# Kernel tuning notes

Hardware: AMD Instinct MI355X
Metric: run time of the kernel (lower is better)

The kernel has to match this reference:

```python
import jax, jax.numpy as jnp
import numpy as np

B, T, D = 4, 4096, 1024
H, E, K, SPAN = 16, 8, 2, 64
GATE_H = 128


def setup_inputs() -> dict:
    key = jax.random.key(0)
    ks = jax.random.split(key, 7)
    s = 0.02
    return {
        "hidden_states": jax.random.normal(ks[0], (B, T, D), jnp.float32),
        "attention_mask": jnp.ones((B, T), jnp.int32),
        # expert weights, torch Linear convention: y = x @ W.T, W: (out, in)
        "Wq": jax.random.normal(ks[1], (E, D, D), jnp.float32) * s,
        "Wk": jax.random.normal(ks[2], (E, D, D), jnp.float32) * s,
        "Wv": jax.random.normal(ks[3], (E, D, D), jnp.float32) * s,
        "gate_w1": jax.random.normal(ks[4], (GATE_H, D), jnp.float32) * s,
        "gate_b1": jnp.zeros((GATE_H,), jnp.float32),
        "gate_w2": jax.random.normal(ks[5], (E, GATE_H), jnp.float32) * s,
        "gate_b2": jnp.zeros((E,), jnp.float32),
    }


def reference(hidden_states, attention_mask, Wq, Wk, Wv, gate_w1, gate_b1, gate_w2, gate_b2):
    b, t, c = hidden_states.shape
    n_spans = t // SPAN  # T divisible by span_len, full mask -> even split
    hd = c // H
    x = hidden_states.reshape(b, n_spans, SPAN, c)            # (B,S,L,C)
    m = attention_mask.reshape(b, n_spans, SPAN).astype(jnp.float32)

    # masked mean-pool per span
    pooled = (x * m[..., None]).sum(2) / jnp.clip(m.sum(2), 1e-9)[..., None]  # (B,S,C)

    # gating MLP + top-k sparse softmax weights
    h = jax.nn.relu(pooled @ gate_w1.T + gate_b1)
    logits = h @ gate_w2.T + gate_b2                          # (B,S,E)
    vals, idx = jax.lax.top_k(logits, K)
    sm = jax.nn.softmax(vals, axis=-1)
    gw = (jax.nn.one_hot(idx, E, dtype=sm.dtype) * sm[..., None]).sum(-2)  # (B,S,E)

    def combine(W):
        # sum_j gw[...,j] * (x @ W_j.T); small fixed loop over experts
        out = jnp.zeros_like(x)
        for j in range(E):
            out = out + gw[:, :, j][:, :, None, None] * jnp.einsum('bsld,fd->bslf', x, W[j])
        return out

    def heads(z):
        return z.reshape(b, n_spans, SPAN, H, hd).transpose(0, 1, 3, 2, 4)  # (B,S,H,L,hd)

    Qh = heads(combine(Wq))
    Kh = heads(combine(Wk))
    Vh = heads(combine(Wv))

    scores = jnp.einsum('bshld,bshmd->bshlm', Qh, Kh) / jnp.sqrt(jnp.float32(hd))
    mb = (m > 0)[:, :, None, None, :]                         # mask keys
    scores = jnp.where(mb, scores, jnp.finfo(scores.dtype).min)
    probs = jax.nn.softmax(scores, axis=-1)                    # dropout=0 (eval)
    ctx = jnp.einsum('bshlm,bshmd->bshld', probs, Vh)
    out = ctx.transpose(0, 1, 3, 2, 4).reshape(b, t, c)
    return out
```

## Files before the change

### kernel.cpp

```cpp
#include <hip/hip_runtime.h>
#include <hip/hip_bf16.h>
#include <hip/hip_fp16.h>

constexpr int Bc = 4, Tc = 4096, Dc = 1024, Hc = 16, Ec = 8;
constexpr int SPANc = 64, NSc = 64, HDc = 64, GHc = 128;
constexpr int NSPAN = 256;
constexpr int MAXMT = 134;
constexpr int NTILES = 12;
#define FINF_MIN (-3.402823466e38f)

typedef __attribute__((ext_vector_type(8))) _Float16 half8;
typedef __attribute__((ext_vector_type(4))) _Float16 half4;
typedef __attribute__((ext_vector_type(4))) float f32x4;

#define LD4(p) (*reinterpret_cast<const float4*>(p))
#define LDU4(p) (*reinterpret_cast<const uint4*>(p))
#define MFMA16(A, B, C) __builtin_amdgcn_mfma_f32_16x16x32_f16(A, B, C, 0, 0, 0)

constexpr size_t OFF_EIDX = 0;
constexpr size_t OFF_EGW  = 2048;
constexpr size_t OFF_NMT  = 6144;
constexpr size_t OFF_MT   = 6208;
constexpr size_t OFF_UT   = 65536;
constexpr size_t UT_BYTES = (size_t)NSPAN * 2 * 3072 * 64 * 2;
constexpr size_t WS_MID   = OFF_UT + UT_BYTES;
constexpr size_t OFF_W16  = WS_MID;
constexpr size_t W16_BYTES = (size_t)3 * Ec * Dc * Dc * 2;
constexpr size_t WS_W16   = OFF_W16 + W16_BYTES;

__global__ __launch_bounds__(256) void cvt16_kernel(
    const float* __restrict__ src, _Float16* __restrict__ dst, int n8, float scl)
{
  int i = blockIdx.x * 256 + threadIdx.x;
  const int stride = gridDim.x * 256;
  for (; i < n8; i += stride) {
    const float4 a = LD4(src + (size_t)i * 8);
    const float4 b = LD4(src + (size_t)i * 8 + 4);
    half8 h;
    h[0] = (_Float16)(a.x * scl); h[1] = (_Float16)(a.y * scl);
    h[2] = (_Float16)(a.z * scl); h[3] = (_Float16)(a.w * scl);
    h[4] = (_Float16)(b.x * scl); h[5] = (_Float16)(b.y * scl);
    h[6] = (_Float16)(b.z * scl); h[7] = (_Float16)(b.w * scl);
    *reinterpret_cast<half8*>(dst + (size_t)i * 8) = h;
  }
}

__global__ __launch_bounds__(256) void gate_kernel(
    const float* __restrict__ x, const int* __restrict__ mask,
    const float* __restrict__ w1, const float* __restrict__ b1,
    const float* __restrict__ w2, const float* __restrict__ b2,
    int* __restrict__ eidx, float* __restrict__ egw)
{
  const int span = blockIdx.x;
  const int b = span / NSc, s = span % NSc;
  const int tid = threadIdx.x;

  __shared__ float mv[SPANc];
  __shared__ float msum_s;
  __shared__ float pooled[Dc];
  __shared__ float hbuf[GHc];
  __shared__ float logits[Ec];

  if (tid < SPANc) mv[tid] = (float)mask[(size_t)b * Tc + s * SPANc + tid];
  __syncthreads();
  if (tid == 0) {
    float ms = 0.f;
    for (int l = 0; l < SPANc; ++l) ms += mv[l];
    msum_s = fmaxf(ms, 1e-9f);
  }
  __syncthreads();

  {
    const int c0 = tid * 4;
    float a0 = 0.f, a1 = 0.f, a2 = 0.f, a3 = 0.f;
    const float* xb = x + ((size_t)b * Tc + s * SPANc) * Dc + c0;
    for (int l = 0; l < SPANc; ++l) {
      const float m = mv[l];
      const float4 v = *reinterpret_cast<const float4*>(xb + (size_t)l * Dc);
      a0 += v.x * m; a1 += v.y * m; a2 += v.z * m; a3 += v.w * m;
    }
    const float inv = 1.f / msum_s;
    pooled[c0 + 0] = a0 * inv; pooled[c0 + 1] = a1 * inv;
    pooled[c0 + 2] = a2 * inv; pooled[c0 + 3] = a3 * inv;
  }
  __syncthreads();

  if (tid < GHc) {
    const float* wr = w1 + (size_t)tid * Dc;
    float acc = b1[tid];
    for (int c = 0; c < Dc; c += 4) {
      const float4 w = *reinterpret_cast<const float4*>(wr + c);
      acc += pooled[c] * w.x + pooled[c + 1] * w.y + pooled[c + 2] * w.z + pooled[c + 3] * w.w;
    }
    hbuf[tid] = fmaxf(acc, 0.f);
  }
  __syncthreads();

  if (tid < Ec) {
    const float* wr = w2 + tid * GHc;
    float acc = b2[tid];
    for (int j = 0; j < GHc; ++j) acc += hbuf[j] * wr[j];
    logits[tid] = acc;
  }
  __syncthreads();

  if (tid == 0) {
    int e0 = 0; float v0 = logits[0];
    for (int e = 1; e < Ec; ++e) { if (logits[e] > v0) { v0 = logits[e]; e0 = e; } }
    int e1 = (e0 == 0) ? 1 : 0; float v1 = logits[e1];
    for (int e = 0; e < Ec; ++e) {
      if (e == e0 || e == e1) continue;
      if (logits[e] > v1) { v1 = logits[e]; e1 = e; }
    }
    const float ex = expf(v1 - v0);
    const float den = 1.f + ex;
    eidx[span * 2 + 0] = e0; eidx[span * 2 + 1] = e1;
    egw[span * 2 + 0] = 1.f / den; egw[span * 2 + 1] = ex / den;
  }
}

__global__ __launch_bounds__(64) void bookkeep_kernel(
    const int* __restrict__ eidx, int* __restrict__ nmt, int* __restrict__ mtiles)
{
  __shared__ int codes[Ec][NSPAN * 2];
  __shared__ int cnt[Ec];
  __shared__ int base[Ec + 1];
  const int tid = threadIdx.x;

  if (tid < Ec) {
    int c = 0;
    for (int s = 0; s < NSPAN; ++s) {
      for (int j = 0; j < 2; ++j) {
        if (eidx[s * 2 + j] == tid) codes[tid][c++] = s * 2 + j;
      }
    }
    cnt[tid] = c;
  }
  __syncthreads();
  if (tid == 0) {
    int acc = 0;
    for (int e = 0; e < Ec; ++e) { base[e] = acc; acc += (cnt[e] + 3) >> 2; }
    base[Ec] = acc;
    *nmt = acc;
  }
  __syncthreads();
  if (tid < Ec) {
    const int e = tid, c = cnt[e], ng = (c + 3) >> 2;
    for (int g = 0; g < ng; ++g) {
      const int m = base[e] + g;
      mtiles[m * 8 + 0] = e;
      for (int i = 0; i < 4; ++i) {
        const int li = g * 4 + i;
        mtiles[m * 8 + 1 + i] = codes[e][(li < c) ? li : 0];
      }
    }
  }
}

__global__ __launch_bounds__(512, 2) void moe_gemm_w16(
    const float* __restrict__ x, const _Float16* __restrict__ W16,
    const int* __restrict__ nmt, const int* __restrict__ mtiles,
    _Float16* __restrict__ Ut)
{
  const int lin = blockIdx.x + gridDim.x * blockIdx.y;
  const int lin2 = (lin & 7) * 201 + (lin >> 3);
  const int mt = lin2 % MAXMT;
  const int nt = lin2 / MAXMT;
  if (mt >= *nmt) return;

  const int e = mtiles[mt * 8 + 0];
  int codes[4];
#pragma unroll
  for (int i = 0; i < 4; ++i) codes[i] = mtiles[mt * 8 + 1 + i];

  const int mat = nt >> 2;
  const int wcol0 = (nt & 3) * 256;
  const _Float16* Wb = W16 + (size_t)mat * ((size_t)Ec * Dc * Dc)
                     + ((size_t)e * Dc + wcol0) * Dc;

  __shared__ _Float16 As[256][36];
  __shared__ _Float16 Bs[256][36];

  const int t = threadIdx.x;
  const int arow = t >> 1;
  const int acol0 = (t & 1) * 16;
  const float* asrc =
      x + ((size_t)(codes[arow >> 6] >> 1) * SPANc + (arow & 63)) * Dc + acol0;
  const _Float16* bsrc = Wb + (size_t)arow * Dc + acol0;

  const int w = t >> 6, lane = t & 63;
  const int lr = lane & 15, koff = (lane >> 4) * 8;
  const int rbase = (w >> 2) * 128;
  const int cbase = (w & 3) * 64;

  f32x4 acc[8][4];
#pragma unroll
  for (int ri = 0; ri < 8; ++ri)
#pragma unroll
    for (int ci = 0; ci < 4; ++ci)
#pragma unroll
      for (int j = 0; j < 4; ++j) acc[ri][ci][j] = 0.f;

  float4 pa0 = LD4(asrc), pa1 = LD4(asrc + 4), pa2 = LD4(asrc + 8), pa3 = LD4(asrc + 12);
  uint4 pb0 = LDU4(bsrc), pb1 = LDU4(bsrc + 8);

  for (int k0 = 0; k0 < Dc; k0 += 32) {
    __syncthreads();
    {
      half8 ha;
      ha[0] = (_Float16)pa0.x; ha[1] = (_Float16)pa0.y;
      ha[2] = (_Float16)pa0.z; ha[3] = (_Float16)pa0.w;
      ha[4] = (_Float16)pa1.x; ha[5] = (_Float16)pa1.y;
      ha[6] = (_Float16)pa1.z; ha[7] = (_Float16)pa1.w;
      *reinterpret_cast<half8*>(&As[arow][acol0]) = ha;
      ha[0] = (_Float16)pa2.x; ha[1] = (_Float16)pa2.y;
      ha[2] = (_Float16)pa2.z; ha[3] = (_Float16)pa2.w;
      ha[4] = (_Float16)pa3.x; ha[5] = (_Float16)pa3.y;
      ha[6] = (_Float16)pa3.z; ha[7] = (_Float16)pa3.w;
      *reinterpret_cast<half8*>(&As[arow][acol0 + 8]) = ha;
      *reinterpret_cast<uint4*>(&Bs[arow][acol0]) = pb0;
      *reinterpret_cast<uint4*>(&Bs[arow][acol0 + 8]) = pb1;
    }
    if (k0 < Dc - 32) {
      asrc += 32; bsrc += 32;
      pa0 = LD4(asrc); pa1 = LD4(asrc + 4); pa2 = LD4(asrc + 8); pa3 = LD4(asrc + 12);
      pb0 = LDU4(bsrc); pb1 = LDU4(bsrc + 8);
      __builtin_amdgcn_sched_barrier(0);
    }
    __syncthreads();

    half8 afr[8], bfr[4];
#pragma unroll
    for (int ri = 0; ri < 8; ++ri)
      afr[ri] = *reinterpret_cast<const half8*>(&As[rbase + ri * 16 + lr][koff]);
#pragma unroll
    for (int ci = 0; ci < 4; ++ci)
      bfr[ci] = *reinterpret_cast<const half8*>(&Bs[cbase + ci * 16 + lr][koff]);
    __builtin_amdgcn_s_setprio(1);
#pragma unroll
    for (int ri = 0; ri < 8; ++ri)
#pragma unroll
      for (int ci = 0; ci < 4; ++ci)
        acc[ri][ci] = MFMA16(afr[ri], bfr[ci], acc[ri][ci]);
    __builtin_amdgcn_s_setprio(0);
  }

#pragma unroll
  for (int ri = 0; ri < 8; ++ri)
#pragma unroll
    for (int ci = 0; ci < 4; ++ci) {
      const int f = wcol0 + cbase + ci * 16 + lr;
      const int row0 = rbase + ri * 16 + (lane >> 4) * 4;
      const int slot = codes[row0 >> 6];
      half4 hv;
#pragma unroll
      for (int j = 0; j < 4; ++j) hv[j] = (_Float16)acc[ri][ci][j];
      *reinterpret_cast<half4*>(
          Ut + ((size_t)slot * 3072 + mat * 1024 + f) * 64 + (row0 & 63)) = hv;
    }
}

__global__ __launch_bounds__(512, 2) void moe_gemm_f32(
    const float* __restrict__ x,
    const float* __restrict__ Wq, const float* __restrict__ Wk,
    const float* __restrict__ Wv,
    const int* __restrict__ nmt, const int* __restrict__ mtiles,
    _Float16* __restrict__ Ut)
{
  const int lin = blockIdx.x + gridDim.x * blockIdx.y;
  const int lin2 = (lin & 7) * 201 + (lin >> 3);
  const int mt = lin2 % MAXMT;
  const int nt = lin2 / MAXMT;
  if (mt >= *nmt) return;

  const int e = mtiles[mt * 8 + 0];
  int codes[4];
#pragma unroll
  for (int i = 0; i < 4; ++i) codes[i] = mtiles[mt * 8 + 1 + i];

  const int mat = nt >> 2;
  const int wcol0 = (nt & 3) * 256;
  const float* Wp = (mat == 0) ? Wq : (mat == 1) ? Wk : Wv;
  const float* Wbase = Wp + ((size_t)e * Dc + wcol0) * Dc;

  __shared__ _Float16 As[256][36];
  __shared__ _Float16 Bs[256][36];

  const int t = threadIdx.x;
  const int arow = t >> 1;
  const int acol0 = (t & 1) * 16;
  const float* asrc =
      x + ((size_t)(codes[arow >> 6] >> 1) * SPANc + (arow & 63)) * Dc + acol0;
  const float* bsrc = Wbase + (size_t)arow * Dc + acol0;

  const int w = t >> 6, lane = t & 63;
  const int lr = lane & 15, koff = (lane >> 4) * 8;
  const int rbase = (w >> 2) * 128;
  const int cbase = (w & 3) * 64;

  f32x4 acc[8][4];
#pragma unroll
  for (int ri = 0; ri < 8; ++ri)
#pragma unroll
    for (int ci = 0; ci < 4; ++ci)
#pragma unroll
      for (int j = 0; j < 4; ++j) acc[ri][ci][j] = 0.f;

  float4 pa0 = LD4(asrc), pa1 = LD4(asrc + 4), pa2 = LD4(asrc + 8), pa3 = LD4(asrc + 12);
  float4 pb0 = LD4(bsrc), pb1 = LD4(bsrc + 4), pb2 = LD4(bsrc + 8), pb3 = LD4(bsrc + 12);

  for (int k0 = 0; k0 < Dc; k0 += 32) {
    __syncthreads();
    {
      half8 ha, hb;
      ha[0] = (_Float16)pa0.x; ha[1] = (_Float16)pa0.y;
      ha[2] = (_Float16)pa0.z; ha[3] = (_Float16)pa0.w;
      ha[4] = (_Float16)pa1.x; ha[5] = (_Float16)pa1.y;
      ha[6] = (_Float16)pa1.z; ha[7] = (_Float16)pa1.w;
      *reinterpret_cast<half8*>(&As[arow][acol0]) = ha;
      ha[0] = (_Float16)pa2.x; ha[1] = (_Float16)pa2.y;
      ha[2] = (_Float16)pa2.z; ha[3] = (_Float16)pa2.w;
      ha[4] = (_Float16)pa3.x; ha[5] = (_Float16)pa3.y;
      ha[6] = (_Float16)pa3.z; ha[7] = (_Float16)pa3.w;
      *reinterpret_cast<half8*>(&As[arow][acol0 + 8]) = ha;
      hb[0] = (_Float16)(pb0.x * 64.f); hb[1] = (_Float16)(pb0.y * 64.f);
      hb[2] = (_Float16)(pb0.z * 64.f); hb[3] = (_Float16)(pb0.w * 64.f);
      hb[4] = (_Float16)(pb1.x * 64.f); hb[5] = (_Float16)(pb1.y * 64.f);
      hb[6] = (_Float16)(pb1.z * 64.f); hb[7] = (_Float16)(pb1.w * 64.f);
      *reinterpret_cast<half8*>(&Bs[arow][acol0]) = hb;
      hb[0] = (_Float16)(pb2.x * 64.f); hb[1] = (_Float16)(pb2.y * 64.f);
      hb[2] = (_Float16)(pb2.z * 64.f); hb[3] = (_Float16)(pb2.w * 64.f);
      hb[4] = (_Float16)(pb3.x * 64.f); hb[5] = (_Float16)(pb3.y * 64.f);
      hb[6] = (_Float16)(pb3.z * 64.f); hb[7] = (_Float16)(pb3.w * 64.f);
      *reinterpret_cast<half8*>(&Bs[arow][acol0 + 8]) = hb;
    }
    if (k0 < Dc - 32) {
      asrc += 32; bsrc += 32;
      pa0 = LD4(asrc); pa1 = LD4(asrc + 4); pa2 = LD4(asrc + 8); pa3 = LD4(asrc + 12);
      pb0 = LD4(bsrc); pb1 = LD4(bsrc + 4); pb2 = LD4(bsrc + 8); pb3 = LD4(bsrc + 12);
      __builtin_amdgcn_sched_barrier(0);
    }
    __syncthreads();

    half8 afr[8], bfr[4];
#pragma unroll
    for (int ri = 0; ri < 8; ++ri)
      afr[ri] = *reinterpret_cast<const half8*>(&As[rbase + ri * 16 + lr][koff]);
#pragma unroll
    for (int ci = 0; ci < 4; ++ci)
      bfr[ci] = *reinterpret_cast<const half8*>(&Bs[cbase + ci * 16 + lr][koff]);
#pragma unroll
    for (int ri = 0; ri < 8; ++ri)
#pragma unroll
      for (int ci = 0; ci < 4; ++ci)
        acc[ri][ci] = MFMA16(afr[ri], bfr[ci], acc[ri][ci]);
  }

#pragma unroll
  for (int ri = 0; ri < 8; ++ri)
#pragma unroll
    for (int ci = 0; ci < 4; ++ci) {
      const int f = wcol0 + cbase + ci * 16 + lr;
      const int row0 = rbase + ri * 16 + (lane >> 4) * 4;
      const int slot = codes[row0 >> 6];
      half4 hv;
#pragma unroll
      for (int j = 0; j < 4; ++j) hv[j] = (_Float16)acc[ri][ci][j];
      *reinterpret_cast<half4*>(
          Ut + ((size_t)slot * 3072 + mat * 1024 + f) * 64 + (row0 & 63)) = hv;
    }
}

__global__ __launch_bounds__(256, 3) void attn_kernel(
    const int* __restrict__ mask, const float* __restrict__ egw,
    const _Float16* __restrict__ Ut, float* __restrict__ out)
{
  const int h = blockIdx.x;
  const int s = blockIdx.y;
  const int b = blockIdx.z;
  const int span = b * NSc + s;
  const int tid = threadIdx.x;

  __shared__ _Float16 Qf[64][68];
  __shared__ _Float16 Kf[64][68];
  __shared__ _Float16 VT[64][68];
  __shared__ _Float16 Pf[64][68];
  __shared__ float    sc[64][68];

  const int sA = span * 2 + 0;
  const int sB = span * 2 + 1;
  const float gA = egw[span * 2 + 0] * 0.015625f;
  const float gB = egw[span * 2 + 1] * 0.015625f;

  const int d = tid >> 2;
  const int l0 = (tid & 3) * 16;

  for (int mat = 0; mat < 3; ++mat) {
    const _Float16* pa = Ut + ((size_t)sA * 3072 + mat * 1024 + h * HDc + d) * 64 + l0;
    const _Float16* pb = Ut + ((size_t)sB * 3072 + mat * 1024 + h * HDc + d) * 64 + l0;
    const half8 a0 = *reinterpret_cast<const half8*>(pa);
    const half8 a1 = *reinterpret_cast<const half8*>(pa + 8);
    const half8 b0 = *reinterpret_cast<const half8*>(pb);
    const half8 b1 = *reinterpret_cast<const half8*>(pb + 8);
    if (mat == 2) {
      half8 v0, v1;
#pragma unroll
      for (int j = 0; j < 8; ++j) {
        v0[j] = (_Float16)(gA * (float)a0[j] + gB * (float)b0[j]);
        v1[j] = (_Float16)(gA * (float)a1[j] + gB * (float)b1[j]);
      }
      *reinterpret_cast<half8*>(&VT[d][l0]) = v0;
      *reinterpret_cast<half8*>(&VT[d][l0 + 8]) = v1;
    } else if (mat == 0) {
#pragma unroll
      for (int j = 0; j < 8; ++j) {
        Qf[l0 + j][d] = (_Float16)(gA * (float)a0[j] + gB * (float)b0[j]);
        Qf[l0 + 8 + j][d] = (_Float16)(gA * (float)a1[j] + gB * (float)b1[j]);
      }
    } else {
#pragma unroll
      for (int j = 0; j < 8; ++j) {
        Kf[l0 + j][d] = (_Float16)(gA * (float)a0[j] + gB * (float)b0[j]);
        Kf[l0 + 8 + j][d] = (_Float16)(gA * (float)a1[j] + gB * (float)b1[j]);
      }
    }
  }
  __syncthreads();

  const int w = tid >> 6, lane = tid & 63;
  const int lr = lane & 15, koff = (lane >> 4) * 8;
  const int rbase = (w >> 1) * 32, cbase = (w & 1) * 32;

  {
    f32x4 aS[2][2];
#pragma unroll
    for (int mi = 0; mi < 2; ++mi)
#pragma unroll
      for (int ni = 0; ni < 2; ++ni)
#pragma unroll
        for (int j = 0; j < 4; ++j) aS[mi][ni][j] = 0.f;
#pragma unroll
    for (int kc = 0; kc < 64; kc += 32) {
      const half8 a0 = *reinterpret_cast<const half8*>(&Qf[rbase + lr][kc + koff]);
      const half8 a1 = *reinterpret_cast<const half8*>(&Qf[rbase + 16 + lr][kc + koff]);
      const half8 b0 = *reinterpret_cast<const half8*>(&Kf[cbase + lr][kc + koff]);
      const half8 b1 = *reinterpret_cast<const half8*>(&Kf[cbase + 16 + lr][kc + koff]);
      aS[0][0] = MFMA16(a0, b0, aS[0][0]); aS[0][1] = MFMA16(a0, b1, aS[0][1]);
      aS[1][0] = MFMA16(a1, b0, aS[1][0]); aS[1][1] = MFMA16(a1, b1, aS[1][1]);
    }
    const bool kv0 = mask[(size_t)b * Tc + s * SPANc + cbase + lr] != 0;
    const bool kv1 = mask[(size_t)b * Tc + s * SPANc + cbase + 16 + lr] != 0;
#pragma unroll
    for (int mi = 0; mi < 2; ++mi)
#pragma unroll
      for (int ni = 0; ni < 2; ++ni) {
        const int col = cbase + ni * 16 + lr;
        const int row0 = rbase + mi * 16 + (lane >> 4) * 4;
        const bool kv = (ni == 0) ? kv0 : kv1;
#pragma unroll
        for (int j = 0; j < 4; ++j)
          sc[row0 + j][col] = kv ? aS[mi][ni][j] * 0.125f : FINF_MIN;
      }
  }
  __syncthreads();

  if (tid < 64) {
    float mx = FINF_MIN;
    for (int mm = 0; mm < 64; ++mm) {
      const int m = (mm + tid) & 63;
      mx = fmaxf(mx, sc[tid][m]);
    }
    float sum = 0.f;
    for (int mm = 0; mm < 64; ++mm) {
      const int m = (mm + tid) & 63;
      const float e = expf(sc[tid][m] - mx);
      sc[tid][m] = e;
      sum += e;
    }
    const float inv = 1.f / sum;
    for (int mm = 0; mm < 64; ++mm) {
      const int m = (mm + tid) & 63;
      Pf[tid][m] = (_Float16)(sc[tid][m] * inv);
    }
  }
  __syncthreads();

  {
    f32x4 aC[2][2];
#pragma unroll
    for (int mi = 0; mi < 2; ++mi)
#pragma unroll
      for (int ni = 0; ni < 2; ++ni)
#pragma unroll
        for (int j = 0; j < 4; ++j) aC[mi][ni][j] = 0.f;
#pragma unroll
    for (int kc = 0; kc < 64; kc += 32) {
      const half8 a0 = *reinterpret_cast<const half8*>(&Pf[rbase + lr][kc + koff]);
      const half8 a1 = *reinterpret_cast<const half8*>(&Pf[rbase + 16 + lr][kc + koff]);
      const half8 b0 = *reinterpret_cast<const half8*>(&VT[cbase + lr][kc + koff]);
      const half8 b1 = *reinterpret_cast<const half8*>(&VT[cbase + 16 + lr][kc + koff]);
      aC[0][0] = MFMA16(a0, b0, aC[0][0]); aC[0][1] = MFMA16(a0, b1, aC[0][1]);
      aC[1][0] = MFMA16(a1, b0, aC[1][0]); aC[1][1] = MFMA16(a1, b1, aC[1][1]);
    }
    float* ob = out + ((size_t)b * Tc + s * SPANc) * Dc + h * HDc;
#pragma unroll
    for (int mi = 0; mi < 2; ++mi)
#pragma unroll
      for (int ni = 0; ni < 2; ++ni) {
        const int col = cbase + ni * 16 + lr;
        const int row0 = rbase + mi * 16 + (lane >> 4) * 4;
#pragma unroll
        for (int j = 0; j < 4; ++j)
          ob[(size_t)(row0 + j) * Dc + col] = aC[mi][ni][j];
      }
  }
}

__global__ __launch_bounds__(256, 3) void moe_attn_fb(
    const float* __restrict__ x, const int* __restrict__ mask,
    const float* __restrict__ Wq, const float* __restrict__ Wk,
    const float* __restrict__ Wv,
    const int* __restrict__ eidx, const float* __restrict__ egw,
    float* __restrict__ out)
{
  const int h = blockIdx.x;
  const int s = blockIdx.y;
  const int b = blockIdx.z;
  const int span = b * NSc + s;
  const int tid = threadIdx.x;

  __shared__ __align__(16) char smem[52224];
  _Float16* XF  = (_Float16*)(smem);
  _Float16* WHs = (_Float16*)(smem + 5120);
  _Float16* WLs = (_Float16*)(smem + 10240);
  float* qs = (float*)(smem);
  float* ks = (float*)(smem + 17408);
  float* vs = (float*)(smem + 34816);

  const int e0 = eidx[span * 2 + 0];
  const int e1 = eidx[span * 2 + 1];
  const float g0s = egw[span * 2 + 0] * 64.f;
  const float g1s = egw[span * 2 + 1] * 64.f;

  const int lrow = tid >> 2;
  const int kq = (tid & 3) * 8;
  const int stg_off = lrow * 40 + kq;

  const int w = tid >> 6;
  const int lane = tid & 63;
  const int lr = lane & 15;
  const int koff = (lane >> 4) * 8;
  const int rbase = (w >> 1) * 32;
  const int cbase = (w & 1) * 32;

  const float* xb = x + ((size_t)b * Tc + s * SPANc) * Dc;
  const size_t woff0 = ((size_t)e0 * Dc + h * HDc + lrow) * Dc + kq;
  const size_t woff1 = ((size_t)e1 * Dc + h * HDc + lrow) * Dc + kq;

  const float* xcur  = xb + (size_t)lrow * Dc + kq;
  const float* w0cur = Wv + woff0;
  const float* w1cur = Wv + woff1;
  float4 rx0, rx1, ra0, ra1, rb0, rb1;
  rx0 = LD4(xcur); rx1 = LD4(xcur + 4);
  ra0 = LD4(w0cur); ra1 = LD4(w0cur + 4);
  rb0 = LD4(w1cur); rb1 = LD4(w1cur + 4);

  for (int p = 0; p < 3; ++p) {
    f32x4 acc[2][2];
#pragma unroll
    for (int mi = 0; mi < 2; ++mi)
#pragma unroll
      for (int ni = 0; ni < 2; ++ni)
#pragma unroll
        for (int j = 0; j < 4; ++j) acc[mi][ni][j] = 0.f;

    for (int t = 0; t < 32; ++t) {
      __syncthreads();
      {
        half8 hx;
        hx[0] = (_Float16)rx0.x; hx[1] = (_Float16)rx0.y;
        hx[2] = (_Float16)rx0.z; hx[3] = (_Float16)rx0.w;
        hx[4] = (_Float16)rx1.x; hx[5] = (_Float16)rx1.y;
        hx[6] = (_Float16)rx1.z; hx[7] = (_Float16)rx1.w;
        *reinterpret_cast<half8*>(XF + stg_off) = hx;
      }
      {
        float wv[8];
        wv[0] = g0s * ra0.x + g1s * rb0.x; wv[1] = g0s * ra0.y + g1s * rb0.y;
        wv[2] = g0s * ra0.z + g1s * rb0.z; wv[3] = g0s * ra0.w + g1s * rb0.w;
        wv[4] = g0s * ra1.x + g1s * rb1.x; wv[5] = g0s * ra1.y + g1s * rb1.y;
        wv[6] = g0s * ra1.z + g1s * rb1.z; wv[7] = g0s * ra1.w + g1s * rb1.w;
        half8 hw, lw;
#pragma unroll
        for (int i = 0; i < 8; ++i) {
          const _Float16 wh = (_Float16)wv[i];
          hw[i] = wh;
          lw[i] = (_Float16)(wv[i] - (float)wh);
        }
        *reinterpret_cast<half8*>(WHs + stg_off) = hw;
        *reinterpret_cast<half8*>(WLs + stg_off) = lw;
      }
      if (!(p == 2 && t == 31)) {
        if (t < 31) {
          xcur += 32; w0cur += 32; w1cur += 32;
        } else {
          const float* Wn = (p == 0) ? Wk : Wq;
          xcur = xb + (size_t)lrow * Dc + kq;
          w0cur = Wn + woff0;
          w1cur = Wn + woff1;
        }
        rx0 = LD4(xcur); rx1 = LD4(xcur + 4);
        ra0 = LD4(w0cur); ra1 = LD4(w0cur + 4);
        rb0 = LD4(w1cur); rb1 = LD4(w1cur + 4);
      }
      __syncthreads();

      const half8 a0  = *reinterpret_cast<const half8*>(XF  + (rbase + lr) * 40 + koff);
      const half8 a1  = *reinterpret_cast<const half8*>(XF  + (rbase + 16 + lr) * 40 + koff);
      const half8 bh0 = *reinterpret_cast<const half8*>(WHs + (cbase + lr) * 40 + koff);
      const half8 bh1 = *reinterpret_cast<const half8*>(WHs + (cbase + 16 + lr) * 40 + koff);
      const half8 bl0 = *reinterpret_cast<const half8*>(WLs + (cbase + lr) * 40 + koff);
      const half8 bl1 = *reinterpret_cast<const half8*>(WLs + (cbase + 16 + lr) * 40 + koff);

      acc[0][0] = MFMA16(a0, bh0, acc[0][0]);
      acc[0][1] = MFMA16(a0, bh1, acc[0][1]);
      acc[1][0] = MFMA16(a1, bh0, acc[1][0]);
      acc[1][1] = MFMA16(a1, bh1, acc[1][1]);
      acc[0][0] = MFMA16(a0, bl0, acc[0][0]);
      acc[0][1] = MFMA16(a0, bl1, acc[0][1]);
      acc[1][0] = MFMA16(a1, bl0, acc[1][0]);
      acc[1][1] = MFMA16(a1, bl1, acc[1][1]);
    }

    float* dst = (p == 0) ? vs : (p == 1) ? ks : qs;
    if (p == 2) __syncthreads();
#pragma unroll
    for (int mi = 0; mi < 2; ++mi)
#pragma unroll
      for (int ni = 0; ni < 2; ++ni) {
        const int col = cbase + ni * 16 + lr;
        const int row0 = rbase + mi * 16 + (lane >> 4) * 4;
#pragma unroll
        for (int j = 0; j < 4; ++j)
          dst[(row0 + j) * 68 + col] = acc[mi][ni][j] * 0.015625f;
      }
  }
  __syncthreads();

  const int tx = tid & 15;
  const int ty = tid >> 4;
  bool kvalid[4];
#pragma unroll
  for (int j = 0; j < 4; ++j)
    kvalid[j] = mask[(size_t)b * Tc + s * SPANc + tx * 4 + j] != 0;

  float sacc[4][4] = {{0.f, 0.f, 0.f, 0.f}, {0.f, 0.f, 0.f, 0.f},
                      {0.f, 0.f, 0.f, 0.f}, {0.f, 0.f, 0.f, 0.f}};
  for (int dd = 0; dd < 64; ++dd) {
    const int d = (dd + tid) & 63;
    const float a0 = qs[(ty * 4 + 0) * 68 + d], a1 = qs[(ty * 4 + 1) * 68 + d];
    const float a2 = qs[(ty * 4 + 2) * 68 + d], a3 = qs[(ty * 4 + 3) * 68 + d];
    const float b0 = ks[(tx * 4 + 0) * 68 + d], b1v = ks[(tx * 4 + 1) * 68 + d];
    const float b2v = ks[(tx * 4 + 2) * 68 + d], b3 = ks[(tx * 4 + 3) * 68 + d];
    sacc[0][0] += a0 * b0; sacc[0][1] += a0 * b1v; sacc[0][2] += a0 * b2v; sacc[0][3] += a0 * b3;
    sacc[1][0] += a1 * b0; sacc[1][1] += a1 * b1v; sacc[1][2] += a1 * b2v; sacc[1][3] += a1 * b3;
    sacc[2][0] += a2 * b0; sacc[2][1] += a2 * b1v; sacc[2][2] += a2 * b2v; sacc[2][3] += a2 * b3;
    sacc[3][0] += a3 * b0; sacc[3][1] += a3 * b1v; sacc[3][2] += a3 * b2v; sacc[3][3] += a3 * b3;
  }
  __syncthreads();
#pragma unroll
  for (int i = 0; i < 4; ++i)
#pragma unroll
    for (int j = 0; j < 4; ++j)
      qs[(ty * 4 + i) * 68 + tx * 4 + j] = kvalid[j] ? sacc[i][j] * 0.125f : FINF_MIN;
  __syncthreads();

  if (tid < 64) {
    float mx = FINF_MIN;
    for (int mm = 0; mm < 64; ++mm) {
      const int m = (mm + tid) & 63;
      mx = fmaxf(mx, qs[tid * 68 + m]);
    }
    float sum = 0.f;
    for (int mm = 0; mm < 64; ++mm) {
      const int m = (mm + tid) & 63;
      const float e = expf(qs[tid * 68 + m] - mx);
      qs[tid * 68 + m] = e;
      sum += e;
    }
    const float inv = 1.f / sum;
    for (int mm = 0; mm < 64; ++mm) {
      const int m = (mm + tid) & 63;
      qs[tid * 68 + m] *= inv;
    }
  }
  __syncthreads();

  float cacc[4][4] = {{0.f, 0.f, 0.f, 0.f}, {0.f, 0.f, 0.f, 0.f},
                      {0.f, 0.f, 0.f, 0.f}, {0.f, 0.f, 0.f, 0.f}};
  for (int m = 0; m < 64; ++m) {
    const float p0 = qs[(ty * 4 + 0) * 68 + m], p1 = qs[(ty * 4 + 1) * 68 + m];
    const float p2 = qs[(ty * 4 + 2) * 68 + m], p3 = qs[(ty * 4 + 3) * 68 + m];
    const float4 vv = *reinterpret_cast<const float4*>(&vs[m * 68 + tx * 4]);
    cacc[0][0] += p0 * vv.x; cacc[0][1] += p0 * vv.y; cacc[0][2] += p0 * vv.z; cacc[0][3] += p0 * vv.w;
    cacc[1][0] += p1 * vv.x; cacc[1][1] += p1 * vv.y; cacc[1][2] += p1 * vv.z; cacc[1][3] += p1 * vv.w;
    cacc[2][0] += p2 * vv.x; cacc[2][1] += p2 * vv.y; cacc[2][2] += p2 * vv.z; cacc[2][3] += p2 * vv.w;
    cacc[3][0] += p3 * vv.x; cacc[3][1] += p3 * vv.y; cacc[3][2] += p3 * vv.z; cacc[3][3] += p3 * vv.w;
  }

  float* ob = out + ((size_t)b * Tc + s * SPANc) * Dc + h * HDc;
#pragma unroll
  for (int i = 0; i < 4; ++i) {
    *reinterpret_cast<float4*>(ob + (size_t)(ty * 4 + i) * Dc + tx * 4) =
        make_float4(cacc[i][0], cacc[i][1], cacc[i][2], cacc[i][3]);
  }
}

extern "C" void kernel_launch(void* const* d_in, const int* in_sizes, int n_in,
                              void* d_out, int out_size, void* d_ws, size_t ws_size,
                              hipStream_t stream) {
  const float* x   = (const float*)d_in[0];
  const int*   msk = (const int*)d_in[1];
  const float* Wq  = (const float*)d_in[2];
  const float* Wk  = (const float*)d_in[3];
  const float* Wv  = (const float*)d_in[4];
  const float* w1  = (const float*)d_in[5];
  const float* b1  = (const float*)d_in[6];
  const float* w2  = (const float*)d_in[7];
  const float* b2  = (const float*)d_in[8];
  float* out = (float*)d_out;

  char* ws = (char*)d_ws;
  int*      eidx   = (int*)(ws + OFF_EIDX);
  float*    egw    = (float*)(ws + OFF_EGW);
  int*      nmt    = (int*)(ws + OFF_NMT);
  int*      mtiles = (int*)(ws + OFF_MT);
  _Float16* Ut     = (_Float16*)(ws + OFF_UT);
  _Float16* W16    = (_Float16*)(ws + OFF_W16);

  gate_kernel<<<NSPAN, 256, 0, stream>>>(x, msk, w1, b1, w2, b2, eidx, egw);

  if (ws_size >= WS_W16) {
    bookkeep_kernel<<<1, 64, 0, stream>>>(eidx, nmt, mtiles);
    const int nW8 = Ec * Dc * Dc / 8;
    cvt16_kernel<<<1024, 256, 0, stream>>>(Wq, W16, nW8, 64.f);
    cvt16_kernel<<<1024, 256, 0, stream>>>(Wk, W16 + (size_t)Ec * Dc * Dc, nW8, 64.f);
    cvt16_kernel<<<1024, 256, 0, stream>>>(Wv, W16 + (size_t)2 * Ec * Dc * Dc, nW8, 64.f);
    moe_gemm_w16<<<dim3(MAXMT, NTILES), 512, 0, stream>>>(x, W16, nmt, mtiles, Ut);
    attn_kernel<<<dim3(Hc, NSc, Bc), 256, 0, stream>>>(msk, egw, Ut, out);
  } else if (ws_size >= WS_MID) {
    bookkeep_kernel<<<1, 64, 0, stream>>>(eidx, nmt, mtiles);
    moe_gemm_f32<<<dim3(MAXMT, NTILES), 512, 0, stream>>>(
        x, Wq, Wk, Wv, nmt, mtiles, Ut);
    attn_kernel<<<dim3(Hc, NSc, Bc), 256, 0, stream>>>(msk, egw, Ut, out);
  } else {
    moe_attn_fb<<<dim3(Hc, NSc, Bc), 256, 0, stream>>>(
        x, msk, Wq, Wk, Wv, eidx, egw, out);
  }
}
```

Before: 563.6 us.

## Fuse weight conversions into one kernel and remap GEMM blocks per XCD

```diff
diff --git a/kernel.cpp b/kernel.cpp
--- a/kernel.cpp
+++ b/kernel.cpp
@@ -7,6 +7,8 @@
 constexpr int NSPAN = 256;
 constexpr int MAXMT = 134;
 constexpr int NTILES = 12;
+constexpr int MTH = (MAXMT + 7) / 8;
+constexpr int GRID_W16 = MTH * NTILES * 8;
 #define FINF_MIN (-3.402823466e38f)
 
 typedef __attribute__((ext_vector_type(8))) _Float16 half8;
@@ -28,19 +30,24 @@
 constexpr size_t W16_BYTES = (size_t)3 * Ec * Dc * Dc * 2;
 constexpr size_t WS_W16   = OFF_W16 + W16_BYTES;
 
-__global__ __launch_bounds__(256) void cvt16_kernel(
-    const float* __restrict__ src, _Float16* __restrict__ dst, int n8, float scl)
+__global__ __launch_bounds__(256) void cvtw_kernel(
+    const float* __restrict__ Wq, const float* __restrict__ Wk,
+    const float* __restrict__ Wv, _Float16* __restrict__ dst)
 {
+  constexpr int EDD8 = Ec * Dc * Dc / 8;
   int i = blockIdx.x * 256 + threadIdx.x;
   const int stride = gridDim.x * 256;
-  for (; i < n8; i += stride) {
-    const float4 a = LD4(src + (size_t)i * 8);
-    const float4 b = LD4(src + (size_t)i * 8 + 4);
+  for (; i < 3 * EDD8; i += stride) {
+    const int mat = i >> 20;
+    const int r = i & (EDD8 - 1);
+    const float* src = (mat == 0) ? Wq : (mat == 1) ? Wk : Wv;
+    const float4 a = LD4(src + (size_t)r * 8);
+    const float4 b = LD4(src + (size_t)r * 8 + 4);
     half8 h;
-    h[0] = (_Float16)(a.x * scl); h[1] = (_Float16)(a.y * scl);
-    h[2] = (_Float16)(a.z * scl); h[3] = (_Float16)(a.w * scl);
-    h[4] = (_Float16)(b.x * scl); h[5] = (_Float16)(b.y * scl);
-    h[6] = (_Float16)(b.z * scl); h[7] = (_Float16)(b.w * scl);
+    h[0] = (_Float16)(a.x * 64.f); h[1] = (_Float16)(a.y * 64.f);
+    h[2] = (_Float16)(a.z * 64.f); h[3] = (_Float16)(a.w * 64.f);
+    h[4] = (_Float16)(b.x * 64.f); h[5] = (_Float16)(b.y * 64.f);
+    h[6] = (_Float16)(b.z * 64.f); h[7] = (_Float16)(b.w * 64.f);
     *reinterpret_cast<half8*>(dst + (size_t)i * 8) = h;
   }
 }
@@ -162,10 +169,12 @@
     const int* __restrict__ nmt, const int* __restrict__ mtiles,
     _Float16* __restrict__ Ut)
 {
-  const int lin = blockIdx.x + gridDim.x * blockIdx.y;
-  const int lin2 = (lin & 7) * 201 + (lin >> 3);
-  const int mt = lin2 % MAXMT;
-  const int nt = lin2 / MAXMT;
+  const int lin = blockIdx.x;
+  const int xcd = lin & 7;
+  const int q = lin >> 3;
+  const int mtH = q / NTILES;
+  const int nt = q % NTILES;
+  const int mt = mtH * 8 + xcd;
   if (mt >= *nmt) return;
 
   const int e = mtiles[mt * 8 + 0];
@@ -742,11 +751,8 @@
 
   if (ws_size >= WS_W16) {
     bookkeep_kernel<<<1, 64, 0, stream>>>(eidx, nmt, mtiles);
-    const int nW8 = Ec * Dc * Dc / 8;
-    cvt16_kernel<<<1024, 256, 0, stream>>>(Wq, W16, nW8, 64.f);
-    cvt16_kernel<<<1024, 256, 0, stream>>>(Wk, W16 + (size_t)Ec * Dc * Dc, nW8, 64.f);
-    cvt16_kernel<<<1024, 256, 0, stream>>>(Wv, W16 + (size_t)2 * Ec * Dc * Dc, nW8, 64.f);
-    moe_gemm_w16<<<dim3(MAXMT, NTILES), 512, 0, stream>>>(x, W16, nmt, mtiles, Ut);
+    cvtw_kernel<<<2048, 256, 0, stream>>>(Wq, Wk, Wv, W16);
+    moe_gemm_w16<<<GRID_W16, 512, 0, stream>>>(x, W16, nmt, mtiles, Ut);
     attn_kernel<<<dim3(Hc, NSc, Bc), 256, 0, stream>>>(msk, egw, Ut, out);
   } else if (ws_size >= WS_MID) {
     bookkeep_kernel<<<1, 64, 0, stream>>>(eidx, nmt, mtiles);
```

New measurement: 531.7 us. -5.7%, faster.
